# Kernel optimization log

Hardware: AMD Instinct MI355X
Metric: run time of the kernel (lower is better)

Reference implementation:

```python
import jax, jax.numpy as jnp
import numpy as np

EMBED_DIM = 1024
HEADS = 16
HEAD_DIM = EMBED_DIM // HEADS
BATCH = 4
SEQ = 1024


def setup_inputs() -> dict:
    key = jax.random.key(0)
    ks = jax.random.split(key, 9)
    s = 1.0 / np.sqrt(HEAD_DIM)
    so = 1.0 / np.sqrt(EMBED_DIM)
    return {
        "values": jax.random.normal(ks[0], (BATCH, SEQ, EMBED_DIM), dtype=jnp.float32),
        "query": jax.random.normal(ks[1], (BATCH, SEQ, EMBED_DIM), dtype=jnp.float32),
        "key": jax.random.normal(ks[2], (BATCH, SEQ, EMBED_DIM), dtype=jnp.float32),
        "mask": jax.random.randint(ks[3], (BATCH, 1, SEQ, SEQ), 0, 2, dtype=jnp.int32),
        "Wv": jax.random.uniform(ks[4], (HEAD_DIM, HEAD_DIM), jnp.float32, -s, s),
        "Wk": jax.random.uniform(ks[5], (HEAD_DIM, HEAD_DIM), jnp.float32, -s, s),
        "Wq": jax.random.uniform(ks[6], (HEAD_DIM, HEAD_DIM), jnp.float32, -s, s),
        "Wo": jax.random.uniform(ks[7], (EMBED_DIM, EMBED_DIM), jnp.float32, -so, so),
        "bo": jax.random.uniform(ks[8], (EMBED_DIM,), jnp.float32, -so, so),
    }


def reference(values, query, key, mask, Wv, Wk, Wq, Wo, bo):
    N, Lq, E = query.shape
    Lk = key.shape[1]
    H, D = HEADS, HEAD_DIM
    # reshape to heads, then per-head shared linear projection (Linear(head_dim, head_dim), no bias)
    v = jnp.einsum('nlhd,ed->nlhe', values.reshape(N, Lk, H, D), Wv)
    k = jnp.einsum('nlhd,ed->nlhe', key.reshape(N, Lk, H, D), Wk)
    q = jnp.einsum('nlhd,ed->nlhe', query.reshape(N, Lq, H, D), Wq)
    # full [N,H,Q,K] scores, scaled by 1/sqrt(embed_dim) as in source
    sim = jnp.einsum('nqhd,nkhd->nhqk', q, k)
    sim = jnp.where(mask == 0, jnp.float32(-1e20), sim)
    attn = jax.nn.softmax(sim / jnp.sqrt(jnp.float32(E)), axis=3)
    out = jnp.einsum('nhqk,nkhd->nqhd', attn, v).reshape(N, Lq, H * D)
    return out @ Wo.T + bo
```

## Files before the change

### kernel.cpp

```cpp
#include <hip/hip_runtime.h>

#define SEQ 1024
#define HEADS 16
#define HD 64
#define EMB 1024

typedef short bf16x8 __attribute__((ext_vector_type(8)));
typedef float f32x4 __attribute__((ext_vector_type(4)));

static __device__ __forceinline__ unsigned short f2bf(float f) {
  unsigned u = __builtin_bit_cast(unsigned, f);
  u += 0x7FFFu + ((u >> 16) & 1u);
  return (unsigned short)(u >> 16);
}

static __device__ __forceinline__ unsigned cvtpk(float a, float b) {
  unsigned r;
  asm("v_cvt_pk_bf16_f32 %0, %1, %2" : "=v"(r) : "v"(a), "v"(b));
  return r;
}

static __device__ __forceinline__ void gload_lds16(const void* g, void* l) {
  __builtin_amdgcn_global_load_lds((const __attribute__((address_space(1))) unsigned int*)g,
                                   (__attribute__((address_space(3))) unsigned int*)l,
                                   16, 0, 0);
}

__global__ __launch_bounds__(256) void k_prep(const int* __restrict__ mask,
                                              const float* __restrict__ Wo,
                                              const float* __restrict__ Wv,
                                              const float* __restrict__ Wq,
                                              const float* __restrict__ Wk,
                                              unsigned long long* __restrict__ mb,
                                              unsigned short* __restrict__ wob,
                                              unsigned short* __restrict__ wb) {
  const unsigned tid = threadIdx.x;
  if (blockIdx.x < 16384) {
    const unsigned gw = blockIdx.x * 4u + (tid >> 6);
    const unsigned lane = tid & 63u;
    const int v = mask[(size_t)gw * 64u + lane];
    const unsigned long long bits = __ballot(v != 0);
    if (lane == 0) {
      const unsigned n = gw >> 14, qrow = (gw >> 4) & 1023u, ktile = gw & 15u;
      mb[((size_t)n * 16 + ktile) * 1024 + qrow] = bits;
    }
  } else if (blockIdx.x < 17408) {
    const unsigned gid = (blockIdx.x - 16384) * 256u + tid;
    const unsigned e = gid >> 8, rem = gid & 255u;
    const unsigned blk = rem >> 4, cc = rem & 15u;
    const float* src = Wo + (size_t)e * 1024 + blk * 64 + cc;
    const unsigned w0 = cvtpk(src[0], src[16]);
    const unsigned w1 = cvtpk(src[32], src[48]);
    *(uint2*)(wob + (size_t)gid * 4) = make_uint2(w0, w1);
  } else {
    #pragma unroll
    for (int t = 0; t < 3; ++t) {
      const float* src = (t == 0) ? Wv : (t == 1) ? Wq : Wk;
      const float sc = (t == 1) ? 0.045084220027786356f : 1.0f;
      const float4 f0 = *(const float4*)(src + tid * 16);
      const float4 f1 = *(const float4*)(src + tid * 16 + 4);
      const float4 f2 = *(const float4*)(src + tid * 16 + 8);
      const float4 f3 = *(const float4*)(src + tid * 16 + 12);
      uint4 u0, u1;
      u0.x = cvtpk(f0.x * sc, f0.y * sc); u0.y = cvtpk(f0.z * sc, f0.w * sc);
      u0.z = cvtpk(f1.x * sc, f1.y * sc); u0.w = cvtpk(f1.z * sc, f1.w * sc);
      u1.x = cvtpk(f2.x * sc, f2.y * sc); u1.y = cvtpk(f2.z * sc, f2.w * sc);
      u1.z = cvtpk(f3.x * sc, f3.y * sc); u1.w = cvtpk(f3.z * sc, f3.w * sc);
      *(uint4*)(wb + t * 4096 + tid * 16) = u0;
      *(uint4*)(wb + t * 4096 + tid * 16 + 8) = u1;
    }
  }
}

__global__ __launch_bounds__(256) void k_proj(const float* __restrict__ values,
                                              const float* __restrict__ query,
                                              const float* __restrict__ key,
                                              const unsigned short* __restrict__ wb,
                                              unsigned short* __restrict__ vb,
                                              unsigned short* __restrict__ qb,
                                              unsigned short* __restrict__ kb) {
  const int lane = threadIdx.x & 63;
  const int c = lane & 15, g = lane >> 4;
  const int wid = blockIdx.x * 4 + (threadIdx.x >> 6);
  const int t = wid >> 12;
  const int rem = wid & 4095;
  const int n = rem >> 10;
  const int h = (rem >> 6) & 15;
  const int lb = rem & 63;

  const float* x; unsigned short* out;
  if (t == 0)      { x = values; out = vb; }
  else if (t == 1) { x = query;  out = qb; }
  else             { x = key;    out = kb; }
  const unsigned short* W = wb + t * 4096;

  bf16x8 a[2];
  const float* xr = x + ((size_t)n * SEQ + lb * 16 + c) * EMB + h * HD;
  #pragma unroll
  for (int ks = 0; ks < 2; ++ks) {
    const float4 f0 = *(const float4*)(xr + ks * 32 + g * 8);
    const float4 f1 = *(const float4*)(xr + ks * 32 + g * 8 + 4);
    uint4 u;
    u.x = cvtpk(f0.x, f0.y); u.y = cvtpk(f0.z, f0.w);
    u.z = cvtpk(f1.x, f1.y); u.w = cvtpk(f1.z, f1.w);
    a[ks] = __builtin_bit_cast(bf16x8, u);
  }

  f32x4 acc[4] = {};
  #pragma unroll
  for (int cb = 0; cb < 4; ++cb) {
    #pragma unroll
    for (int ks = 0; ks < 2; ++ks) {
      const bf16x8 b = *(const bf16x8*)(W + (cb * 16 + c) * HD + ks * 32 + g * 8);
      acc[cb] = __builtin_amdgcn_mfma_f32_16x16x32_bf16(a[ks], b, acc[cb], 0, 0, 0);
    }
  }

  if (t == 0) {
    unsigned short* vt = out + (size_t)(n * HEADS + h) * (HD * SEQ);
    const int key0 = lb * 16 + 4 * g;
    #pragma unroll
    for (int cb = 0; cb < 4; ++cb) {
      const unsigned w0 = cvtpk(acc[cb][0], acc[cb][1]);
      const unsigned w1 = cvtpk(acc[cb][2], acc[cb][3]);
      *(uint2*)(vt + (size_t)(cb * 16 + c) * SEQ + key0) = make_uint2(w0, w1);
    }
  } else {
    unsigned short* op = out + ((size_t)(n * HEADS + h) * SEQ + lb * 16) * HD;
    #pragma unroll
    for (int r = 0; r < 4; ++r) {
      const unsigned w0 = cvtpk(acc[0][r], acc[1][r]);
      const unsigned w1 = cvtpk(acc[2][r], acc[3][r]);
      *(uint2*)(op + (4 * g + r) * HD + 4 * c) = make_uint2(w0, w1);
    }
  }
}

__global__ __launch_bounds__(256, 4) void k_attn(const unsigned short* __restrict__ qb,
                                                 const unsigned short* __restrict__ kb,
                                                 const unsigned short* __restrict__ vb,
                                                 const unsigned long long* __restrict__ mb,
                                                 unsigned short* __restrict__ ob) {
  const int tid = threadIdx.x;
  const int lane = tid & 63;
  const int c = lane & 15, g = lane >> 4;
  const int bid = blockIdx.x;
  const int nh = bid & 63, q64 = bid >> 6;
  const int n = nh >> 4, h = nh & 15;
  const int qlo = q64 * 64 + (tid >> 6) * 16;

  __shared__ unsigned short Ks[2][64][64];
  __shared__ unsigned short Vs[2][64][64];

  char* const Kb0 = (char*)&Ks[0][0][0];
  char* const Vb0 = (char*)&Vs[0][0][0];

  const size_t nhb = (size_t)(n * HEADS + h) * (SEQ * HD);
  const unsigned short* qp = qb + nhb;
  const char* kpB = (const char*)(kb + nhb);
  const char* vpB = (const char*)(vb + nhb);

  const char* kSrc[2]; const char* vSrc[2]; int ldsOff[2];
  #pragma unroll
  for (int i = 0; i < 2; ++i) {
    const int off = i * 4096 + tid * 16;
    const int row = off >> 7, slot = (off >> 4) & 7;
    const int krow = ((row >> 4) & 1) * 32 + ((row >> 5) & 1) * 4 +
                     ((row >> 2) & 3) * 8 + (row & 3);
    const int sw = (slot ^ (row & 7)) << 4;
    kSrc[i] = kpB + krow * 128 + sw;
    vSrc[i] = vpB + (size_t)row * 2048 + sw;
    ldsOff[i] = off;
  }

  bf16x8 qa[2];
  #pragma unroll
  for (int ks = 0; ks < 2; ++ks)
    qa[ks] = *(const bf16x8*)(qp + (size_t)(qlo + c) * HD + ks * 32 + g * 8);

  bf16x8 ones;
  #pragma unroll
  for (int j = 0; j < 8; ++j) ones[j] = (short)0x3F80;

  f32x4 o[4] = {};
  f32x4 lacc = {};

#define STAGEKV(dstK, dstV, kt_) do {                                   \
    _Pragma("unroll")                                                   \
    for (int i = 0; i < 2; ++i) {                                       \
      gload_lds16(kSrc[i] + (size_t)(kt_) * 8192, (dstK) + ldsOff[i]);  \
      gload_lds16(vSrc[i] + (kt_) * 128, (dstV) + ldsOff[i]);           \
    }                                                                   \
  } while (0)

  STAGEKV(Kb0, Vb0, 0);

  for (int kt = 0; kt < 16; ++kt) {
    const int cur = kt & 1;
    char* const Kc = Kb0 + cur * 8192;
    char* const Vc = Vb0 + cur * 8192;
    if (kt < 15) {
      STAGEKV(Kb0 + (cur ^ 1) * 8192, Vb0 + (cur ^ 1) * 8192, kt + 1);
      asm volatile("s_waitcnt vmcnt(4)" ::: "memory");
    } else {
      asm volatile("s_waitcnt vmcnt(0)" ::: "memory");
    }
    asm volatile("s_barrier" ::: "memory");

    const unsigned long long bits = mb[((size_t)(n * 16 + kt)) * 1024 + qlo + c];
    const unsigned blo = (unsigned)bits, bhi = (unsigned)(bits >> 32);

    bf16x8 kf[4][2];
    #pragma unroll
    for (int sub = 0; sub < 4; ++sub) {
      const int rho = sub * 16 + c;
      #pragma unroll
      for (int ks = 0; ks < 2; ++ks)
        kf[sub][ks] = *(const bf16x8*)(Kc + rho * 128 + (((ks * 4 + g) ^ (c & 7)) << 4));
    }

    f32x4 s[4];
    __builtin_amdgcn_s_setprio(1);
    #pragma unroll
    for (int sub = 0; sub < 4; ++sub) {
      f32x4 acc = {};
      acc = __builtin_amdgcn_mfma_f32_16x16x32_bf16(kf[sub][0], qa[0], acc, 0, 0, 0);
      acc = __builtin_amdgcn_mfma_f32_16x16x32_bf16(kf[sub][1], qa[1], acc, 0, 0, 0);
      s[sub] = acc;
    }
    __builtin_amdgcn_s_setprio(0);

    bf16x8 vf[4][2];
    #pragma unroll
    for (int db = 0; db < 4; ++db) {
      const int row = db * 16 + c;
      #pragma unroll
      for (int ks = 0; ks < 2; ++ks)
        vf[db][ks] = *(const bf16x8*)(Vc + row * 128 + (((ks * 4 + g) ^ (c & 7)) << 4));
    }

    unsigned pw[2][4];
    #pragma unroll
    for (int sub = 0; sub < 4; ++sub) {
      const unsigned x = ((sub & 1) ? bhi : blo) >> (8 * g + ((sub >> 1) << 2));
      const float p0 = (x & 1u) ? __builtin_exp2f(s[sub][0]) : 0.f;
      const float p1 = (x & 2u) ? __builtin_exp2f(s[sub][1]) : 0.f;
      const float p2 = (x & 4u) ? __builtin_exp2f(s[sub][2]) : 0.f;
      const float p3 = (x & 8u) ? __builtin_exp2f(s[sub][3]) : 0.f;
      pw[sub & 1][(sub >> 1) * 2 + 0] = cvtpk(p0, p1);
      pw[sub & 1][(sub >> 1) * 2 + 1] = cvtpk(p2, p3);
    }
    bf16x8 pa[2];
    pa[0] = __builtin_bit_cast(bf16x8, *(uint4*)&pw[0][0]);
    pa[1] = __builtin_bit_cast(bf16x8, *(uint4*)&pw[1][0]);

    __builtin_amdgcn_s_setprio(1);
    #pragma unroll
    for (int ks = 0; ks < 2; ++ks) {
      #pragma unroll
      for (int db = 0; db < 4; ++db)
        o[db] = __builtin_amdgcn_mfma_f32_16x16x32_bf16(pa[ks], vf[db][ks], o[db], 0, 0, 0);
      lacc = __builtin_amdgcn_mfma_f32_16x16x32_bf16(pa[ks], ones, lacc, 0, 0, 0);
    }
    __builtin_amdgcn_s_setprio(0);

    if (kt < 15) asm volatile("s_barrier" ::: "memory");
  }
#undef STAGEKV

  #pragma unroll
  for (int r = 0; r < 4; ++r) {
    const float inv = 1.0f / lacc[r];
    const unsigned w0 = cvtpk(o[0][r] * inv, o[1][r] * inv);
    const unsigned w1 = cvtpk(o[2][r] * inv, o[3][r] * inv);
    *(uint2*)(ob + ((size_t)n * SEQ + qlo + 4 * g + r) * EMB + h * 64 + 4 * c) =
        make_uint2(w0, w1);
  }
}

__global__ __launch_bounds__(256, 4) void k_gemm(const unsigned short* __restrict__ A,
                                                 const unsigned short* __restrict__ B,
                                                 const float* __restrict__ bo,
                                                 float* __restrict__ C) {
  const int tid = threadIdx.x;
  const int w = tid >> 6, lane = tid & 63;
  const int c = lane & 15, g = lane >> 4;
  const int bm = blockIdx.x & 63, bn = blockIdx.x >> 6;
  const int m0 = bm * 64, n0 = bn * 64;
  const int wr = w >> 1, wc = w & 1;

  __shared__ unsigned short As[2][64][64];
  __shared__ unsigned short Bs[2][64][64];

  const char* aSrc[2]; const char* bSrc[2]; int ldsOff[2];
  #pragma unroll
  for (int i = 0; i < 2; ++i) {
    const int off = i * 4096 + tid * 16;
    const int row = off >> 7, slot = (off >> 4) & 7;
    const int sw = (slot ^ (row & 7)) << 4;
    aSrc[i] = (const char*)A + (size_t)(m0 + row) * 2048 + sw;
    bSrc[i] = (const char*)B + (size_t)(n0 + row) * 2048 + sw;
    ldsOff[i] = off;
  }

  f32x4 acc[2][2] = {};

#define STAGE(buf, kt_) do {                                                  \
    _Pragma("unroll")                                                         \
    for (int i = 0; i < 2; ++i) {                                             \
      gload_lds16(aSrc[i] + (kt_) * 128, (char*)&As[buf][0][0] + ldsOff[i]);  \
      gload_lds16(bSrc[i] + (kt_) * 128, (char*)&Bs[buf][0][0] + ldsOff[i]);  \
    }                                                                         \
  } while (0)

  STAGE(0, 0);

  for (int kt = 0; kt < 16; ++kt) {
    const int cur = kt & 1;
    if (kt < 15) {
      STAGE(cur ^ 1, kt + 1);
      asm volatile("s_waitcnt vmcnt(4)" ::: "memory");
    } else {
      asm volatile("s_waitcnt vmcnt(0)" ::: "memory");
    }
    asm volatile("s_barrier" ::: "memory");

    #pragma unroll
    for (int ks = 0; ks < 2; ++ks) {
      bf16x8 af[2], bf_[2];
      #pragma unroll
      for (int i = 0; i < 2; ++i) {
        const int row = wr * 32 + i * 16 + c;
        af[i] = *(const bf16x8*)((char*)&As[cur][0][0] + row * 128 +
                                 (((ks * 4 + g) ^ (c & 7)) << 4));
      }
      #pragma unroll
      for (int j = 0; j < 2; ++j) {
        const int row = wc * 32 + j * 16 + c;
        bf_[j] = *(const bf16x8*)((char*)&Bs[cur][0][0] + row * 128 +
                                  (((ks * 4 + g) ^ (c & 7)) << 4));
      }
      __builtin_amdgcn_s_setprio(1);
      #pragma unroll
      for (int i = 0; i < 2; ++i)
        #pragma unroll
        for (int j = 0; j < 2; ++j)
          acc[i][j] = __builtin_amdgcn_mfma_f32_16x16x32_bf16(af[i], bf_[j], acc[i][j], 0, 0, 0);
      __builtin_amdgcn_s_setprio(0);
    }

    if (kt < 15) asm volatile("s_barrier" ::: "memory");
  }
#undef STAGE

  #pragma unroll
  for (int j = 0; j < 2; ++j) {
    const int col = n0 + wc * 32 + j * 16 + c;
    const float bv = bo[col];
    #pragma unroll
    for (int i = 0; i < 2; ++i) {
      const int rowb = m0 + wr * 32 + i * 16 + 4 * g;
      #pragma unroll
      for (int r = 0; r < 4; ++r)
        C[(size_t)(rowb + r) * 1024 + col] = acc[i][j][r] + bv;
    }
  }
}

extern "C" void kernel_launch(void* const* d_in, const int* in_sizes, int n_in,
                              void* d_out, int out_size, void* d_ws, size_t ws_size,
                              hipStream_t stream) {
  const float* values = (const float*)d_in[0];
  const float* query  = (const float*)d_in[1];
  const float* key    = (const float*)d_in[2];
  const int*   mask   = (const int*)d_in[3];
  const float* Wv     = (const float*)d_in[4];
  const float* Wk     = (const float*)d_in[5];
  const float* Wq     = (const float*)d_in[6];
  const float* Wo     = (const float*)d_in[7];
  const float* bo     = (const float*)d_in[8];
  float* out = (float*)d_out;

  char* ws = (char*)d_ws;
  unsigned short* qb = (unsigned short*)(ws);
  unsigned short* kb = (unsigned short*)(ws + (size_t)8 * 1024 * 1024);
  unsigned short* vb = (unsigned short*)(ws + (size_t)16 * 1024 * 1024);
  unsigned short* ob = (unsigned short*)(ws + (size_t)24 * 1024 * 1024);
  unsigned long long* mb = (unsigned long long*)(ws + (size_t)32 * 1024 * 1024);
  unsigned short* wb  = (unsigned short*)(ws + (size_t)32 * 1024 * 1024 + 512 * 1024);
  unsigned short* wob = (unsigned short*)(ws + (size_t)33 * 1024 * 1024);

  k_prep<<<17409, 256, 0, stream>>>(mask, Wo, Wv, Wq, Wk, mb, wob, wb);
  k_proj<<<3072, 256, 0, stream>>>(values, query, key, wb, vb, qb, kb);
  k_attn<<<1024, 256, 0, stream>>>(qb, kb, vb, mb, ob);
  k_gemm<<<1024, 256, 0, stream>>>(ob, wob, bo, out);
}
```

Baseline: 87.40 us.

## Merge prep and projection kernels, enlarge attention and output GEMM tiles

Fuses the mask packing, Wo conversion and per-head QKV projection into one launch. Each projection block now converts its small weight matrix into LDS itself, which removes a kernel launch and a workspace round trip. The mask-packing blocks each handle four rows per wave. The attention kernel now processes 128 queries per block, 32 per wave, staging two K/V tiles per step so each K/V load is reused twice. The output GEMM moves to 128x64 tiles, with occupancy hints lowered to 2 blocks per CU. In exchange this uses more registers and LDS, launches fewer blocks (512), and repeats the weight conversion in every projection block.

```diff
diff --git a/kernel.cpp b/kernel.cpp
--- a/kernel.cpp
+++ b/kernel.cpp
@@ -8,12 +8,6 @@
 typedef short bf16x8 __attribute__((ext_vector_type(8)));
 typedef float f32x4 __attribute__((ext_vector_type(4)));
 
-static __device__ __forceinline__ unsigned short f2bf(float f) {
-  unsigned u = __builtin_bit_cast(unsigned, f);
-  u += 0x7FFFu + ((u >> 16) & 1u);
-  return (unsigned short)(u >> 16);
-}
-
 static __device__ __forceinline__ unsigned cvtpk(float a, float b) {
   unsigned r;
   asm("v_cvt_pk_bf16_f32 %0, %1, %2" : "=v"(r) : "v"(a), "v"(b));
@@ -26,291 +20,325 @@
                                    16, 0, 0);
 }
 
-__global__ __launch_bounds__(256) void k_prep(const int* __restrict__ mask,
-                                              const float* __restrict__ Wo,
-                                              const float* __restrict__ Wv,
-                                              const float* __restrict__ Wq,
-                                              const float* __restrict__ Wk,
-                                              unsigned long long* __restrict__ mb,
-                                              unsigned short* __restrict__ wob,
-                                              unsigned short* __restrict__ wb) {
+__global__ __launch_bounds__(256) void k_pp(const int* __restrict__ mask,
+                                            const float* __restrict__ Wo,
+                                            const float* __restrict__ Wv,
+                                            const float* __restrict__ Wq,
+                                            const float* __restrict__ Wk,
+                                            const float* __restrict__ values,
+                                            const float* __restrict__ query,
+                                            const float* __restrict__ key,
+                                            unsigned long long* __restrict__ mb,
+                                            unsigned short* __restrict__ wob,
+                                            unsigned short* __restrict__ vb,
+                                            unsigned short* __restrict__ qb,
+                                            unsigned short* __restrict__ kb) {
+  __shared__ unsigned short Wl[64][64];
   const unsigned tid = threadIdx.x;
-  if (blockIdx.x < 16384) {
-    const unsigned gw = blockIdx.x * 4u + (tid >> 6);
+  const unsigned b = blockIdx.x;
+
+  if (b < 3072) {
+    const int lane = tid & 63, c = lane & 15, g = lane >> 4;
+    const int wid = b * 4 + (tid >> 6);
+    const int t = wid >> 12;
+    const int rem = wid & 4095;
+    const int n = rem >> 10, h = (rem >> 6) & 15, lb = rem & 63;
+
+    const float* x; unsigned short* out;
+    if (t == 0)      { x = values; out = vb; }
+    else if (t == 1) { x = query;  out = qb; }
+    else             { x = key;    out = kb; }
+    const float* Wf = (t == 0) ? Wv : (t == 1) ? Wq : Wk;
+    const float sc = (t == 1) ? 0.045084220027786356f : 1.0f;
+
+    {
+      const int row = tid >> 2, c0 = (tid & 3) * 16;
+      const float4 f0 = *(const float4*)(Wf + row * 64 + c0);
+      const float4 f1 = *(const float4*)(Wf + row * 64 + c0 + 4);
+      const float4 f2 = *(const float4*)(Wf + row * 64 + c0 + 8);
+      const float4 f3 = *(const float4*)(Wf + row * 64 + c0 + 12);
+      uint4 u0, u1;
+      u0.x = cvtpk(f0.x * sc, f0.y * sc); u0.y = cvtpk(f0.z * sc, f0.w * sc);
+      u0.z = cvtpk(f1.x * sc, f1.y * sc); u0.w = cvtpk(f1.z * sc, f1.w * sc);
+      u1.x = cvtpk(f2.x * sc, f2.y * sc); u1.y = cvtpk(f2.z * sc, f2.w * sc);
+      u1.z = cvtpk(f3.x * sc, f3.y * sc); u1.w = cvtpk(f3.z * sc, f3.w * sc);
+      const int s0 = ((c0 >> 3) ^ (row & 7)) << 4;
+      const int s1 = (((c0 >> 3) + 1) ^ (row & 7)) << 4;
+      *(uint4*)((char*)&Wl[0][0] + row * 128 + s0) = u0;
+      *(uint4*)((char*)&Wl[0][0] + row * 128 + s1) = u1;
+    }
+    __syncthreads();
+
+    bf16x8 bfr[4][2];
+    #pragma unroll
+    for (int cb = 0; cb < 4; ++cb) {
+      const int row = cb * 16 + c;
+      #pragma unroll
+      for (int ks = 0; ks < 2; ++ks)
+        bfr[cb][ks] = *(const bf16x8*)((char*)&Wl[0][0] + row * 128 +
+                                       (((ks * 4 + g) ^ (c & 7)) << 4));
+    }
+
+    bf16x8 a[2];
+    const float* xr = x + ((size_t)n * SEQ + lb * 16 + c) * EMB + h * HD;
+    #pragma unroll
+    for (int ks = 0; ks < 2; ++ks) {
+      const float4 f0 = *(const float4*)(xr + ks * 32 + g * 8);
+      const float4 f1 = *(const float4*)(xr + ks * 32 + g * 8 + 4);
+      uint4 u;
+      u.x = cvtpk(f0.x, f0.y); u.y = cvtpk(f0.z, f0.w);
+      u.z = cvtpk(f1.x, f1.y); u.w = cvtpk(f1.z, f1.w);
+      a[ks] = __builtin_bit_cast(bf16x8, u);
+    }
+
+    f32x4 acc[4] = {};
+    #pragma unroll
+    for (int cb = 0; cb < 4; ++cb)
+      #pragma unroll
+      for (int ks = 0; ks < 2; ++ks)
+        acc[cb] = __builtin_amdgcn_mfma_f32_16x16x32_bf16(a[ks], bfr[cb][ks], acc[cb], 0, 0, 0);
+
+    if (t == 0) {
+      unsigned short* vt = out + (size_t)(n * HEADS + h) * (HD * SEQ);
+      const int key0 = lb * 16 + 4 * g;
+      #pragma unroll
+      for (int cb = 0; cb < 4; ++cb) {
+        const unsigned w0 = cvtpk(acc[cb][0], acc[cb][1]);
+        const unsigned w1 = cvtpk(acc[cb][2], acc[cb][3]);
+        *(uint2*)(vt + (size_t)(cb * 16 + c) * SEQ + key0) = make_uint2(w0, w1);
+      }
+    } else {
+      unsigned short* op = out + ((size_t)(n * HEADS + h) * SEQ + lb * 16) * HD;
+      #pragma unroll
+      for (int r = 0; r < 4; ++r) {
+        const unsigned w0 = cvtpk(acc[0][r], acc[1][r]);
+        const unsigned w1 = cvtpk(acc[2][r], acc[3][r]);
+        *(uint2*)(op + (4 * g + r) * HD + 4 * c) = make_uint2(w0, w1);
+      }
+    }
+  } else if (b < 7168) {
     const unsigned lane = tid & 63u;
-    const int v = mask[(size_t)gw * 64u + lane];
-    const unsigned long long bits = __ballot(v != 0);
-    if (lane == 0) {
-      const unsigned n = gw >> 14, qrow = (gw >> 4) & 1023u, ktile = gw & 15u;
-      mb[((size_t)n * 16 + ktile) * 1024 + qrow] = bits;
-    }
-  } else if (blockIdx.x < 17408) {
-    const unsigned gid = (blockIdx.x - 16384) * 256u + tid;
+    const unsigned gwb = (b - 3072) * 16u + (tid >> 6) * 4u;
+    #pragma unroll
+    for (int it = 0; it < 4; ++it) {
+      const unsigned gw = gwb + it;
+      const int v = mask[(size_t)gw * 64u + lane];
+      const unsigned long long bits = __ballot(v != 0);
+      if (lane == 0) {
+        const unsigned n = gw >> 14, qrow = (gw >> 4) & 1023u, ktile = gw & 15u;
+        mb[((size_t)n * 16 + ktile) * 1024 + qrow] = bits;
+      }
+    }
+  } else {
+    const unsigned gid = (b - 7168) * 256u + tid;
     const unsigned e = gid >> 8, rem = gid & 255u;
     const unsigned blk = rem >> 4, cc = rem & 15u;
     const float* src = Wo + (size_t)e * 1024 + blk * 64 + cc;
     const unsigned w0 = cvtpk(src[0], src[16]);
     const unsigned w1 = cvtpk(src[32], src[48]);
     *(uint2*)(wob + (size_t)gid * 4) = make_uint2(w0, w1);
-  } else {
-    #pragma unroll
-    for (int t = 0; t < 3; ++t) {
-      const float* src = (t == 0) ? Wv : (t == 1) ? Wq : Wk;
-      const float sc = (t == 1) ? 0.045084220027786356f : 1.0f;
-      const float4 f0 = *(const float4*)(src + tid * 16);
-      const float4 f1 = *(const float4*)(src + tid * 16 + 4);
-      const float4 f2 = *(const float4*)(src + tid * 16 + 8);
-      const float4 f3 = *(const float4*)(src + tid * 16 + 12);
-      uint4 u0, u1;
-      u0.x = cvtpk(f0.x * sc, f0.y * sc); u0.y = cvtpk(f0.z * sc, f0.w * sc);
-      u0.z = cvtpk(f1.x * sc, f1.y * sc); u0.w = cvtpk(f1.z * sc, f1.w * sc);
-      u1.x = cvtpk(f2.x * sc, f2.y * sc); u1.y = cvtpk(f2.z * sc, f2.w * sc);
-      u1.z = cvtpk(f3.x * sc, f3.y * sc); u1.w = cvtpk(f3.z * sc, f3.w * sc);
-      *(uint4*)(wb + t * 4096 + tid * 16) = u0;
-      *(uint4*)(wb + t * 4096 + tid * 16 + 8) = u1;
-    }
-  }
-}
-
-__global__ __launch_bounds__(256) void k_proj(const float* __restrict__ values,
-                                              const float* __restrict__ query,
-                                              const float* __restrict__ key,
-                                              const unsigned short* __restrict__ wb,
-                                              unsigned short* __restrict__ vb,
-                                              unsigned short* __restrict__ qb,
-                                              unsigned short* __restrict__ kb) {
-  const int lane = threadIdx.x & 63;
-  const int c = lane & 15, g = lane >> 4;
-  const int wid = blockIdx.x * 4 + (threadIdx.x >> 6);
-  const int t = wid >> 12;
-  const int rem = wid & 4095;
-  const int n = rem >> 10;
-  const int h = (rem >> 6) & 15;
-  const int lb = rem & 63;
-
-  const float* x; unsigned short* out;
-  if (t == 0)      { x = values; out = vb; }
-  else if (t == 1) { x = query;  out = qb; }
-  else             { x = key;    out = kb; }
-  const unsigned short* W = wb + t * 4096;
-
-  bf16x8 a[2];
-  const float* xr = x + ((size_t)n * SEQ + lb * 16 + c) * EMB + h * HD;
-  #pragma unroll
-  for (int ks = 0; ks < 2; ++ks) {
-    const float4 f0 = *(const float4*)(xr + ks * 32 + g * 8);
-    const float4 f1 = *(const float4*)(xr + ks * 32 + g * 8 + 4);
-    uint4 u;
-    u.x = cvtpk(f0.x, f0.y); u.y = cvtpk(f0.z, f0.w);
-    u.z = cvtpk(f1.x, f1.y); u.w = cvtpk(f1.z, f1.w);
-    a[ks] = __builtin_bit_cast(bf16x8, u);
-  }
-
-  f32x4 acc[4] = {};
-  #pragma unroll
-  for (int cb = 0; cb < 4; ++cb) {
-    #pragma unroll
-    for (int ks = 0; ks < 2; ++ks) {
-      const bf16x8 b = *(const bf16x8*)(W + (cb * 16 + c) * HD + ks * 32 + g * 8);
-      acc[cb] = __builtin_amdgcn_mfma_f32_16x16x32_bf16(a[ks], b, acc[cb], 0, 0, 0);
-    }
-  }
-
-  if (t == 0) {
-    unsigned short* vt = out + (size_t)(n * HEADS + h) * (HD * SEQ);
-    const int key0 = lb * 16 + 4 * g;
-    #pragma unroll
-    for (int cb = 0; cb < 4; ++cb) {
-      const unsigned w0 = cvtpk(acc[cb][0], acc[cb][1]);
-      const unsigned w1 = cvtpk(acc[cb][2], acc[cb][3]);
-      *(uint2*)(vt + (size_t)(cb * 16 + c) * SEQ + key0) = make_uint2(w0, w1);
-    }
-  } else {
-    unsigned short* op = out + ((size_t)(n * HEADS + h) * SEQ + lb * 16) * HD;
-    #pragma unroll
-    for (int r = 0; r < 4; ++r) {
-      const unsigned w0 = cvtpk(acc[0][r], acc[1][r]);
-      const unsigned w1 = cvtpk(acc[2][r], acc[3][r]);
-      *(uint2*)(op + (4 * g + r) * HD + 4 * c) = make_uint2(w0, w1);
-    }
-  }
-}
-
-__global__ __launch_bounds__(256, 4) void k_attn(const unsigned short* __restrict__ qb,
+  }
+}
+
+__global__ __launch_bounds__(256, 2) void k_attn(const unsigned short* __restrict__ qb,
                                                  const unsigned short* __restrict__ kb,
                                                  const unsigned short* __restrict__ vb,
                                                  const unsigned long long* __restrict__ mb,
                                                  unsigned short* __restrict__ ob) {
   const int tid = threadIdx.x;
-  const int lane = tid & 63;
+  const int w = tid >> 6, lane = tid & 63;
   const int c = lane & 15, g = lane >> 4;
   const int bid = blockIdx.x;
-  const int nh = bid & 63, q64 = bid >> 6;
+  const int nh = bid & 63, q128 = bid >> 6;
   const int n = nh >> 4, h = nh & 15;
-  const int qlo = q64 * 64 + (tid >> 6) * 16;
-
-  __shared__ unsigned short Ks[2][64][64];
-  __shared__ unsigned short Vs[2][64][64];
-
-  char* const Kb0 = (char*)&Ks[0][0][0];
-  char* const Vb0 = (char*)&Vs[0][0][0];
+  const int qlo = q128 * 128 + w * 32;
+
+  __shared__ unsigned short Ks[2][2][64][64];
+  __shared__ unsigned short Vs[2][2][64][64];
+
+  char* const Kb0 = (char*)&Ks[0][0][0][0];
+  char* const Vb0 = (char*)&Vs[0][0][0][0];
 
   const size_t nhb = (size_t)(n * HEADS + h) * (SEQ * HD);
   const unsigned short* qp = qb + nhb;
   const char* kpB = (const char*)(kb + nhb);
   const char* vpB = (const char*)(vb + nhb);
 
-  const char* kSrc[2]; const char* vSrc[2]; int ldsOff[2];
-  #pragma unroll
-  for (int i = 0; i < 2; ++i) {
+  const char* kSrc[4]; const char* vSrc[4]; int ldsOff[4];
+  #pragma unroll
+  for (int i = 0; i < 4; ++i) {
     const int off = i * 4096 + tid * 16;
-    const int row = off >> 7, slot = (off >> 4) & 7;
-    const int krow = ((row >> 4) & 1) * 32 + ((row >> 5) & 1) * 4 +
-                     ((row >> 2) & 3) * 8 + (row & 3);
-    const int sw = (slot ^ (row & 7)) << 4;
-    kSrc[i] = kpB + krow * 128 + sw;
-    vSrc[i] = vpB + (size_t)row * 2048 + sw;
+    const int row = off >> 7;
+    const int tile = row >> 6, r64 = row & 63;
+    const int slot = (off >> 4) & 7;
+    const int krow = ((r64 >> 4) & 1) * 32 + ((r64 >> 5) & 1) * 4 +
+                     ((r64 >> 2) & 3) * 8 + (r64 & 3);
+    const int sw = (slot ^ (r64 & 7)) << 4;
+    kSrc[i] = kpB + (size_t)(tile * 64 + krow) * 128 + sw;
+    vSrc[i] = vpB + (size_t)r64 * 2048 + tile * 128 + sw;
     ldsOff[i] = off;
   }
 
-  bf16x8 qa[2];
-  #pragma unroll
-  for (int ks = 0; ks < 2; ++ks)
-    qa[ks] = *(const bf16x8*)(qp + (size_t)(qlo + c) * HD + ks * 32 + g * 8);
+  bf16x8 qa[2][2];
+  #pragma unroll
+  for (int grp = 0; grp < 2; ++grp)
+    #pragma unroll
+    for (int ks = 0; ks < 2; ++ks)
+      qa[grp][ks] = *(const bf16x8*)(qp + (size_t)(qlo + grp * 16 + c) * HD + ks * 32 + g * 8);
 
   bf16x8 ones;
   #pragma unroll
   for (int j = 0; j < 8; ++j) ones[j] = (short)0x3F80;
 
-  f32x4 o[4] = {};
-  f32x4 lacc = {};
-
-#define STAGEKV(dstK, dstV, kt_) do {                                   \
-    _Pragma("unroll")                                                   \
-    for (int i = 0; i < 2; ++i) {                                       \
-      gload_lds16(kSrc[i] + (size_t)(kt_) * 8192, (dstK) + ldsOff[i]);  \
-      gload_lds16(vSrc[i] + (kt_) * 128, (dstV) + ldsOff[i]);           \
-    }                                                                   \
+  f32x4 o[2][4] = {};
+  f32x4 lacc[2] = {};
+
+#define STAGEKV(dstK, dstV, kp_) do {                                    \
+    _Pragma("unroll")                                                    \
+    for (int i = 0; i < 4; ++i) {                                        \
+      gload_lds16(kSrc[i] + (size_t)(kp_) * 16384, (dstK) + ldsOff[i]);  \
+      gload_lds16(vSrc[i] + (kp_) * 256, (dstV) + ldsOff[i]);            \
+    }                                                                    \
   } while (0)
 
   STAGEKV(Kb0, Vb0, 0);
 
-  for (int kt = 0; kt < 16; ++kt) {
-    const int cur = kt & 1;
-    char* const Kc = Kb0 + cur * 8192;
-    char* const Vc = Vb0 + cur * 8192;
-    if (kt < 15) {
-      STAGEKV(Kb0 + (cur ^ 1) * 8192, Vb0 + (cur ^ 1) * 8192, kt + 1);
-      asm volatile("s_waitcnt vmcnt(4)" ::: "memory");
+  for (int kp = 0; kp < 8; ++kp) {
+    const int cur = kp & 1;
+    if (kp < 7) {
+      STAGEKV(Kb0 + (cur ^ 1) * 16384, Vb0 + (cur ^ 1) * 16384, kp + 1);
+      asm volatile("s_waitcnt vmcnt(8)" ::: "memory");
     } else {
       asm volatile("s_waitcnt vmcnt(0)" ::: "memory");
     }
     asm volatile("s_barrier" ::: "memory");
 
-    const unsigned long long bits = mb[((size_t)(n * 16 + kt)) * 1024 + qlo + c];
-    const unsigned blo = (unsigned)bits, bhi = (unsigned)(bits >> 32);
-
-    bf16x8 kf[4][2];
-    #pragma unroll
-    for (int sub = 0; sub < 4; ++sub) {
-      const int rho = sub * 16 + c;
-      #pragma unroll
-      for (int ks = 0; ks < 2; ++ks)
-        kf[sub][ks] = *(const bf16x8*)(Kc + rho * 128 + (((ks * 4 + g) ^ (c & 7)) << 4));
-    }
-
-    f32x4 s[4];
-    __builtin_amdgcn_s_setprio(1);
-    #pragma unroll
-    for (int sub = 0; sub < 4; ++sub) {
-      f32x4 acc = {};
-      acc = __builtin_amdgcn_mfma_f32_16x16x32_bf16(kf[sub][0], qa[0], acc, 0, 0, 0);
-      acc = __builtin_amdgcn_mfma_f32_16x16x32_bf16(kf[sub][1], qa[1], acc, 0, 0, 0);
-      s[sub] = acc;
-    }
-    __builtin_amdgcn_s_setprio(0);
-
-    bf16x8 vf[4][2];
-    #pragma unroll
-    for (int db = 0; db < 4; ++db) {
-      const int row = db * 16 + c;
-      #pragma unroll
-      for (int ks = 0; ks < 2; ++ks)
-        vf[db][ks] = *(const bf16x8*)(Vc + row * 128 + (((ks * 4 + g) ^ (c & 7)) << 4));
-    }
-
-    unsigned pw[2][4];
-    #pragma unroll
-    for (int sub = 0; sub < 4; ++sub) {
-      const unsigned x = ((sub & 1) ? bhi : blo) >> (8 * g + ((sub >> 1) << 2));
-      const float p0 = (x & 1u) ? __builtin_exp2f(s[sub][0]) : 0.f;
-      const float p1 = (x & 2u) ? __builtin_exp2f(s[sub][1]) : 0.f;
-      const float p2 = (x & 4u) ? __builtin_exp2f(s[sub][2]) : 0.f;
-      const float p3 = (x & 8u) ? __builtin_exp2f(s[sub][3]) : 0.f;
-      pw[sub & 1][(sub >> 1) * 2 + 0] = cvtpk(p0, p1);
-      pw[sub & 1][(sub >> 1) * 2 + 1] = cvtpk(p2, p3);
-    }
-    bf16x8 pa[2];
-    pa[0] = __builtin_bit_cast(bf16x8, *(uint4*)&pw[0][0]);
-    pa[1] = __builtin_bit_cast(bf16x8, *(uint4*)&pw[1][0]);
-
-    __builtin_amdgcn_s_setprio(1);
-    #pragma unroll
-    for (int ks = 0; ks < 2; ++ks) {
-      #pragma unroll
-      for (int db = 0; db < 4; ++db)
-        o[db] = __builtin_amdgcn_mfma_f32_16x16x32_bf16(pa[ks], vf[db][ks], o[db], 0, 0, 0);
-      lacc = __builtin_amdgcn_mfma_f32_16x16x32_bf16(pa[ks], ones, lacc, 0, 0, 0);
-    }
-    __builtin_amdgcn_s_setprio(0);
-
-    if (kt < 15) asm volatile("s_barrier" ::: "memory");
+    #pragma unroll
+    for (int t = 0; t < 2; ++t) {
+      const int kt = kp * 2 + t;
+      char* const Kc = Kb0 + cur * 16384 + t * 8192;
+      char* const Vc = Vb0 + cur * 16384 + t * 8192;
+
+      const unsigned long long bits0 = mb[((size_t)(n * 16 + kt)) * 1024 + qlo + c];
+      const unsigned long long bits1 = mb[((size_t)(n * 16 + kt)) * 1024 + qlo + 16 + c];
+
+      bf16x8 kf[4][2];
+      #pragma unroll
+      for (int sub = 0; sub < 4; ++sub) {
+        const int rho = sub * 16 + c;
+        #pragma unroll
+        for (int ks = 0; ks < 2; ++ks)
+          kf[sub][ks] = *(const bf16x8*)(Kc + rho * 128 + (((ks * 4 + g) ^ (c & 7)) << 4));
+      }
+      bf16x8 vf[4][2];
+      #pragma unroll
+      for (int db = 0; db < 4; ++db) {
+        const int row = db * 16 + c;
+        #pragma unroll
+        for (int ks = 0; ks < 2; ++ks)
+          vf[db][ks] = *(const bf16x8*)(Vc + row * 128 + (((ks * 4 + g) ^ (c & 7)) << 4));
+      }
+
+      #pragma unroll
+      for (int grp = 0; grp < 2; ++grp) {
+        const unsigned long long bits = grp ? bits1 : bits0;
+        const unsigned blo = (unsigned)bits, bhi = (unsigned)(bits >> 32);
+
+        f32x4 s[4];
+        __builtin_amdgcn_s_setprio(1);
+        #pragma unroll
+        for (int sub = 0; sub < 4; ++sub) {
+          f32x4 acc = {};
+          acc = __builtin_amdgcn_mfma_f32_16x16x32_bf16(kf[sub][0], qa[grp][0], acc, 0, 0, 0);
+          acc = __builtin_amdgcn_mfma_f32_16x16x32_bf16(kf[sub][1], qa[grp][1], acc, 0, 0, 0);
+          s[sub] = acc;
+        }
+        __builtin_amdgcn_s_setprio(0);
+
+        unsigned pw[2][4];
+        #pragma unroll
+        for (int sub = 0; sub < 4; ++sub) {
+          const unsigned x = ((sub & 1) ? bhi : blo) >> (8 * g + ((sub >> 1) << 2));
+          const float p0 = (x & 1u) ? __builtin_exp2f(s[sub][0]) : 0.f;
+          const float p1 = (x & 2u) ? __builtin_exp2f(s[sub][1]) : 0.f;
+          const float p2 = (x & 4u) ? __builtin_exp2f(s[sub][2]) : 0.f;
+          const float p3 = (x & 8u) ? __builtin_exp2f(s[sub][3]) : 0.f;
+          pw[sub & 1][(sub >> 1) * 2 + 0] = cvtpk(p0, p1);
+          pw[sub & 1][(sub >> 1) * 2 + 1] = cvtpk(p2, p3);
+        }
+        bf16x8 pa[2];
+        pa[0] = __builtin_bit_cast(bf16x8, *(uint4*)&pw[0][0]);
+        pa[1] = __builtin_bit_cast(bf16x8, *(uint4*)&pw[1][0]);
+
+        __builtin_amdgcn_s_setprio(1);
+        #pragma unroll
+        for (int ks = 0; ks < 2; ++ks) {
+          #pragma unroll
+          for (int db = 0; db < 4; ++db)
+            o[grp][db] = __builtin_amdgcn_mfma_f32_16x16x32_bf16(pa[ks], vf[db][ks], o[grp][db], 0, 0, 0);
+          lacc[grp] = __builtin_amdgcn_mfma_f32_16x16x32_bf16(pa[ks], ones, lacc[grp], 0, 0, 0);
+        }
+        __builtin_amdgcn_s_setprio(0);
+      }
+    }
+
+    if (kp < 7) asm volatile("s_barrier" ::: "memory");
   }
 #undef STAGEKV
 
   #pragma unroll
-  for (int r = 0; r < 4; ++r) {
-    const float inv = 1.0f / lacc[r];
-    const unsigned w0 = cvtpk(o[0][r] * inv, o[1][r] * inv);
-    const unsigned w1 = cvtpk(o[2][r] * inv, o[3][r] * inv);
-    *(uint2*)(ob + ((size_t)n * SEQ + qlo + 4 * g + r) * EMB + h * 64 + 4 * c) =
-        make_uint2(w0, w1);
-  }
-}
-
-__global__ __launch_bounds__(256, 4) void k_gemm(const unsigned short* __restrict__ A,
+  for (int grp = 0; grp < 2; ++grp)
+    #pragma unroll
+    for (int r = 0; r < 4; ++r) {
+      const float inv = 1.0f / lacc[grp][r];
+      const unsigned w0 = cvtpk(o[grp][0][r] * inv, o[grp][1][r] * inv);
+      const unsigned w1 = cvtpk(o[grp][2][r] * inv, o[grp][3][r] * inv);
+      *(uint2*)(ob + ((size_t)n * SEQ + qlo + grp * 16 + 4 * g + r) * EMB + h * 64 + 4 * c) =
+          make_uint2(w0, w1);
+    }
+}
+
+__global__ __launch_bounds__(256, 2) void k_gemm(const unsigned short* __restrict__ A,
                                                  const unsigned short* __restrict__ B,
                                                  const float* __restrict__ bo,
                                                  float* __restrict__ C) {
   const int tid = threadIdx.x;
   const int w = tid >> 6, lane = tid & 63;
   const int c = lane & 15, g = lane >> 4;
-  const int bm = blockIdx.x & 63, bn = blockIdx.x >> 6;
-  const int m0 = bm * 64, n0 = bn * 64;
-  const int wr = w >> 1, wc = w & 1;
-
-  __shared__ unsigned short As[2][64][64];
+  const int bm = blockIdx.x & 31, bn = blockIdx.x >> 5;
+  const int m0 = bm * 128, n0 = bn * 64;
+
+  __shared__ unsigned short As[2][128][64];
   __shared__ unsigned short Bs[2][64][64];
 
-  const char* aSrc[2]; const char* bSrc[2]; int ldsOff[2];
+  const char* aSrc[4]; int aOff[4];
+  const char* bSrc[2]; int bOff[2];
+  #pragma unroll
+  for (int i = 0; i < 4; ++i) {
+    const int off = i * 4096 + tid * 16;
+    const int row = off >> 7, slot = (off >> 4) & 7;
+    const int sw = (slot ^ (row & 7)) << 4;
+    aSrc[i] = (const char*)A + (size_t)(m0 + row) * 2048 + sw;
+    aOff[i] = off;
+  }
   #pragma unroll
   for (int i = 0; i < 2; ++i) {
     const int off = i * 4096 + tid * 16;
     const int row = off >> 7, slot = (off >> 4) & 7;
     const int sw = (slot ^ (row & 7)) << 4;
-    aSrc[i] = (const char*)A + (size_t)(m0 + row) * 2048 + sw;
     bSrc[i] = (const char*)B + (size_t)(n0 + row) * 2048 + sw;
-    ldsOff[i] = off;
-  }
-
-  f32x4 acc[2][2] = {};
+    bOff[i] = off;
+  }
+
+  f32x4 acc[2][4] = {};
 
 #define STAGE(buf, kt_) do {                                                  \
     _Pragma("unroll")                                                         \
-    for (int i = 0; i < 2; ++i) {                                             \
-      gload_lds16(aSrc[i] + (kt_) * 128, (char*)&As[buf][0][0] + ldsOff[i]);  \
-      gload_lds16(bSrc[i] + (kt_) * 128, (char*)&Bs[buf][0][0] + ldsOff[i]);  \
-    }                                                                         \
+    for (int i = 0; i < 4; ++i)                                               \
+      gload_lds16(aSrc[i] + (kt_) * 128, (char*)&As[buf][0][0] + aOff[i]);    \
+    _Pragma("unroll")                                                         \
+    for (int i = 0; i < 2; ++i)                                               \
+      gload_lds16(bSrc[i] + (kt_) * 128, (char*)&Bs[buf][0][0] + bOff[i]);    \
   } while (0)
 
   STAGE(0, 0);
@@ -319,7 +347,7 @@
     const int cur = kt & 1;
     if (kt < 15) {
       STAGE(cur ^ 1, kt + 1);
-      asm volatile("s_waitcnt vmcnt(4)" ::: "memory");
+      asm volatile("s_waitcnt vmcnt(6)" ::: "memory");
     } else {
       asm volatile("s_waitcnt vmcnt(0)" ::: "memory");
     }
@@ -327,16 +355,16 @@
 
     #pragma unroll
     for (int ks = 0; ks < 2; ++ks) {
-      bf16x8 af[2], bf_[2];
+      bf16x8 af[2], bf_[4];
       #pragma unroll
       for (int i = 0; i < 2; ++i) {
-        const int row = wr * 32 + i * 16 + c;
+        const int row = w * 32 + i * 16 + c;
         af[i] = *(const bf16x8*)((char*)&As[cur][0][0] + row * 128 +
                                  (((ks * 4 + g) ^ (c & 7)) << 4));
       }
       #pragma unroll
-      for (int j = 0; j < 2; ++j) {
-        const int row = wc * 32 + j * 16 + c;
+      for (int j = 0; j < 4; ++j) {
+        const int row = j * 16 + c;
         bf_[j] = *(const bf16x8*)((char*)&Bs[cur][0][0] + row * 128 +
                                   (((ks * 4 + g) ^ (c & 7)) << 4));
       }
@@ -344,7 +372,7 @@
       #pragma unroll
       for (int i = 0; i < 2; ++i)
         #pragma unroll
-        for (int j = 0; j < 2; ++j)
+        for (int j = 0; j < 4; ++j)
           acc[i][j] = __builtin_amdgcn_mfma_f32_16x16x32_bf16(af[i], bf_[j], acc[i][j], 0, 0, 0);
       __builtin_amdgcn_s_setprio(0);
     }
@@ -354,12 +382,12 @@
 #undef STAGE
 
   #pragma unroll
-  for (int j = 0; j < 2; ++j) {
-    const int col = n0 + wc * 32 + j * 16 + c;
+  for (int j = 0; j < 4; ++j) {
+    const int col = n0 + j * 16 + c;
     const float bv = bo[col];
     #pragma unroll
     for (int i = 0; i < 2; ++i) {
-      const int rowb = m0 + wr * 32 + i * 16 + 4 * g;
+      const int rowb = m0 + w * 32 + i * 16 + 4 * g;
       #pragma unroll
       for (int r = 0; r < 4; ++r)
         C[(size_t)(rowb + r) * 1024 + col] = acc[i][j][r] + bv;
@@ -387,11 +415,9 @@
   unsigned short* vb = (unsigned short*)(ws + (size_t)16 * 1024 * 1024);
   unsigned short* ob = (unsigned short*)(ws + (size_t)24 * 1024 * 1024);
   unsigned long long* mb = (unsigned long long*)(ws + (size_t)32 * 1024 * 1024);
-  unsigned short* wb  = (unsigned short*)(ws + (size_t)32 * 1024 * 1024 + 512 * 1024);
   unsigned short* wob = (unsigned short*)(ws + (size_t)33 * 1024 * 1024);
 
-  k_prep<<<17409, 256, 0, stream>>>(mask, Wo, Wv, Wq, Wk, mb, wob, wb);
-  k_proj<<<3072, 256, 0, stream>>>(values, query, key, wb, vb, qb, kb);
-  k_attn<<<1024, 256, 0, stream>>>(qb, kb, vb, mb, ob);
-  k_gemm<<<1024, 256, 0, stream>>>(ob, wob, bo, out);
-}
+  k_pp<<<8192, 256, 0, stream>>>(mask, Wo, Wv, Wq, Wk, values, query, key, mb, wob, vb, qb, kb);
+  k_attn<<<512, 256, 0, stream>>>(qb, kb, vb, mb, ob);
+  k_gemm<<<512, 256, 0, stream>>>(ob, wob, bo, out);
+}
```

Result: faster. 76.77 us (-12.2%).
